# Optimization experiments

Measured on AMD Instinct MI355X. Metric: run time of the kernel, lower is better.

Reference implementation:

```python
import jax, jax.numpy as jnp
import numpy as np

B, C, T, H, F, KS = 8, 512, 1024, 8, 2048, 3
K = C // H            # head channels = 64
ROPE_D = K // 2       # RoPE rotates half the head channels = 32
EPS = 1e-4


def setup_inputs() -> dict:
    key = jax.random.key(0)
    ks = jax.random.split(key, 12)
    s = 1.0 / np.sqrt(C)
    sf = 1.0 / np.sqrt(F)
    return {
        "x": jax.random.normal(ks[0], (B, C, T), jnp.float32),
        "x_mask": jnp.ones((B, 1, T), jnp.float32),
        "attn_mask": jnp.ones((B, 1, T, T), jnp.float32),
        "wq": jax.random.normal(ks[1], (C, C), jnp.float32) * s,
        "bq": jnp.zeros((C,), jnp.float32),
        "wk": jax.random.normal(ks[2], (C, C), jnp.float32) * s,
        "bk": jnp.zeros((C,), jnp.float32),
        "wv": jax.random.normal(ks[3], (C, C), jnp.float32) * s,
        "bv": jnp.zeros((C,), jnp.float32),
        "wo": jax.random.normal(ks[4], (C, C), jnp.float32) * s,
        "bo": jnp.zeros((C,), jnp.float32),
        "w1": jax.random.normal(ks[5], (F, C, KS), jnp.float32) * s,
        "b1": jnp.zeros((F,), jnp.float32),
        "w2": jax.random.normal(ks[6], (C, F, KS), jnp.float32) * sf,
        "b2": jnp.zeros((C,), jnp.float32),
        "g1": jnp.ones((C,), jnp.float32),
        "be1": jnp.zeros((C,), jnp.float32),
        "g2": jnp.ones((C,), jnp.float32),
        "be2": jnp.zeros((C,), jnp.float32),
    }


def _rope(x):
    # x: (B, H, T, K); rotate first ROPE_D channels, pass the rest through.
    t = x.shape[2]
    theta = 1.0 / (10000.0 ** (jnp.arange(0, ROPE_D, 2, dtype=jnp.float32) / ROPE_D))
    idx = jnp.arange(t, dtype=jnp.float32)[:, None] * theta[None, :]  # (T, d/2)
    idx2 = jnp.concatenate([idx, idx], axis=-1)                       # (T, d)
    cos, sin = jnp.cos(idx2), jnp.sin(idx2)                           # broadcast over B,H
    xr, xp = x[..., :ROPE_D], x[..., ROPE_D:]
    h = ROPE_D // 2
    neg = jnp.concatenate([-xr[..., h:], xr[..., :h]], axis=-1)
    return jnp.concatenate([xr * cos + neg * sin, xp], axis=-1)


def _ln(x, gamma, beta):
    # channel-wise LayerNorm over dim 1 of (B, C, T), eps=1e-4
    mean = jnp.mean(x, axis=1, keepdims=True)
    var = jnp.mean((x - mean) ** 2, axis=1, keepdims=True)
    xn = (x - mean) * jax.lax.rsqrt(var + EPS)
    return xn * gamma[None, :, None] + beta[None, :, None]


def _conv1d(x, w, b):
    # x: (B, Cin, T), w: (Cout, Cin, KS), 'same' padding (KS//2)
    y = jax.lax.conv_general_dilated(
        x, w, window_strides=(1,), padding=[(KS // 2, KS // 2)],
        dimension_numbers=("NCH", "OIH", "NCH"))
    return y + b[None, :, None]


def _forward(x, x_mask, attn_mask, wq, bq, wk, bk, wv, bv, wo, bo,
             w1, b1, w2, b2, g1, be1, g2, be2):
    x = x * x_mask
    # 1x1 conv projections == channel matmuls
    q = jnp.einsum("oc,bct->bot", wq, x) + bq[None, :, None]
    k = jnp.einsum("oc,bct->bot", wk, x) + bk[None, :, None]
    v = jnp.einsum("oc,bct->bot", wv, x) + bv[None, :, None]
    # (B, C, T) -> (B, H, T, K)
    def heads(a):
        return a.reshape(B, H, K, T).transpose(0, 1, 3, 2)
    q, k, v = heads(q), heads(k), heads(v)
    q = _rope(q)
    k = _rope(k)
    scores = jnp.einsum("bhtk,bhsk->bhts", q, k) / jnp.sqrt(jnp.float32(K))
    scores = jnp.where(attn_mask == 0, jnp.float32(-10000.0), scores)
    p = jax.nn.softmax(scores, axis=-1)
    o = jnp.einsum("bhts,bhsk->bhtk", p, v)              # (B,H,T,K)
    o = o.transpose(0, 1, 3, 2).reshape(B, C, T)
    y = jnp.einsum("oc,bct->bot", wo, o) + bo[None, :, None]
    x = _ln(x + y, g1, be1)
    # conv FFN
    h1 = jax.nn.relu(_conv1d(x * x_mask, w1, b1))
    y = _conv1d(h1 * x_mask, w2, b2) * x_mask
    x = _ln(x + y, g2, be2)
    return x


def reference(x, x_mask, attn_mask, wq, bq, wk, bk, wv, bv, wo, bo,
              w1, b1, w2, b2, g1, be1, g2, be2):
    return _forward(x, x_mask, attn_mask, wq, bq, wk, bk, wv, bv, wo, bo,
                    w1, b1, w2, b2, g1, be1, g2, be2)
```

## Files before the change

kernel.cpp:

```cpp
#include <hip/hip_runtime.h>

typedef unsigned short u16;
typedef __attribute__((ext_vector_type(4))) float floatx4;
typedef __attribute__((ext_vector_type(8))) __bf16 bf16x8;
typedef __attribute__((ext_vector_type(4))) unsigned short ushort4v;
typedef __attribute__((ext_vector_type(8))) unsigned short ushort8v;

#define DI __device__ __forceinline__


DI u16 f2bf(float f) {
  union { float f; unsigned u; } v; v.f = f;
  unsigned r = v.u + 0x7fffu + ((v.u >> 16) & 1u);
  return (u16)(r >> 16);
}
DI float bf2f(u16 h) {
  union { unsigned u; float f; } v; v.u = ((unsigned)h) << 16;
  return v.f;
}

#define GLDS(g, l) __builtin_amdgcn_global_load_lds( \
    (const __attribute__((address_space(1))) unsigned int*)(g), \
    (__attribute__((address_space(3))) unsigned int*)(l), 16, 0, 0)

__global__ __launch_bounds__(256, 2) void k_fattn(
    const u16* __restrict__ qb, const u16* __restrict__ kb,
    const u16* __restrict__ vb, const unsigned* __restrict__ mb,
    u16* __restrict__ oT)
{
  __shared__ __align__(16) u16 Ps[4][32 * 64];
  const int tid  = threadIdx.x;
  const int wave = tid >> 6, lane = tid & 63;
  const int lr = lane & 15, kg = lane >> 4;
  const int qt = blockIdx.x, bh = blockIdx.y;
  const int bb = bh >> 3, hh = bh & 7;
  const int wq0 = qt * 128 + wave * 32;
  const float L2E = 1.44269504f;

  const u16* Qp = qb + (size_t)bh * 65536;
  const u16* Kp = kb + (size_t)bh * 65536;
  const u16* Vp = vb + (size_t)bh * 65536;
  u16* Pw = &Ps[wave][0];

  bf16x8 qf[2][2];
#pragma unroll
  for (int i = 0; i < 2; ++i)
#pragma unroll
    for (int h = 0; h < 2; ++h)
      qf[i][h] = *(const bf16x8*)&Qp[(wq0 + i * 16 + lr) * 64 + h * 32 + kg * 8];

  float l_b[2] = {0.f, 0.f};
  floatx4 o_acc[2][4];
#pragma unroll
  for (int i = 0; i < 2; ++i)
#pragma unroll
    for (int j = 0; j < 4; ++j) o_acc[i][j] = (floatx4){0.f, 0.f, 0.f, 0.f};

  bf16x8 kf[4][2], vf[4][2];
#pragma unroll
  for (int a = 0; a < 4; ++a)
#pragma unroll
    for (int h = 0; h < 2; ++h)
      kf[a][h] = *(const bf16x8*)&Kp[(a * 16 + lr) * 64 + h * 32 + kg * 8];

  for (int it = 0; it < 16; ++it) {
    const int s0 = it * 64;
    unsigned mw[2][2];
#pragma unroll
    for (int b = 0; b < 2; ++b) {
      const size_t rw = ((size_t)bb << 15) + ((size_t)(wq0 + b * 16 + lr) << 5) + (s0 >> 5);
      mw[b][0] = mb[rw]; mw[b][1] = mb[rw + 1];
    }
    floatx4 sT[4][2];
    __builtin_amdgcn_s_setprio(1);
#pragma unroll
    for (int a = 0; a < 4; ++a) {
      sT[a][0] = (floatx4){0.f, 0.f, 0.f, 0.f};
      sT[a][1] = (floatx4){0.f, 0.f, 0.f, 0.f};
#pragma unroll
      for (int b = 0; b < 2; ++b)
#pragma unroll
        for (int h = 0; h < 2; ++h)
          sT[a][b] = __builtin_amdgcn_mfma_f32_16x16x32_bf16(kf[a][h], qf[b][h], sT[a][b], 0, 0, 0);
    }
    __builtin_amdgcn_s_setprio(0);
#pragma unroll
    for (int a = 0; a < 4; ++a)
#pragma unroll
      for (int h = 0; h < 2; ++h)
        vf[a][h] = *(const bf16x8*)&Vp[(a * 16 + lr) * 1024 + s0 + h * 32 + kg * 8];
    if (it < 15) {
      const int sn = s0 + 64;
#pragma unroll
      for (int a = 0; a < 4; ++a)
#pragma unroll
        for (int h = 0; h < 2; ++h)
          kf[a][h] = *(const bf16x8*)&Kp[(sn + a * 16 + lr) * 64 + h * 32 + kg * 8];
    }
#pragma unroll
    for (int b = 0; b < 2; ++b) {
      float sum = 0.f;
#pragma unroll
      for (int a = 0; a < 4; ++a)
#pragma unroll
        for (int r = 0; r < 4; ++r) {
          const int sl = a * 16 + kg * 4 + r;
          float sv = sT[a][b][r] * 0.125f;
          const unsigned wsel = (sl & 32) ? mw[b][1] : mw[b][0];
          if (!((wsel >> (sl & 31)) & 1u)) sv = -10000.f;
          const float p = exp2f(sv * L2E);
          sT[a][b][r] = p;
          sum += p;
        }
      sum += __shfl_xor(sum, 16);
      sum += __shfl_xor(sum, 32);
      l_b[b] += sum;
#pragma unroll
      for (int a = 0; a < 4; ++a) {
        ushort4v pk;
#pragma unroll
        for (int r = 0; r < 4; ++r) {
          __bf16 hv = (__bf16)sT[a][b][r];
          pk[r] = *(u16*)&hv;
        }
        const int sl0 = a * 16 + kg * 4;
        *(ushort4v*)&Pw[(b * 16 + lr) * 64 + (sl0 ^ ((lr & 7) << 3))] = pk;
      }
    }
    asm volatile("s_waitcnt lgkmcnt(0)" ::: "memory");
    __builtin_amdgcn_sched_barrier(0);
    bf16x8 pa[2][2];
#pragma unroll
    for (int i = 0; i < 2; ++i)
#pragma unroll
      for (int h = 0; h < 2; ++h)
        pa[i][h] = *(const bf16x8*)&Pw[(i * 16 + lr) * 64 + (((h * 4 + kg) ^ (lr & 7)) << 3)];
    __builtin_amdgcn_s_setprio(1);
#pragma unroll
    for (int jd = 0; jd < 4; ++jd)
#pragma unroll
      for (int i = 0; i < 2; ++i)
#pragma unroll
        for (int h = 0; h < 2; ++h)
          o_acc[i][jd] = __builtin_amdgcn_mfma_f32_16x16x32_bf16(pa[i][h], vf[jd][h], o_acc[i][jd], 0, 0, 0);
    __builtin_amdgcn_s_setprio(0);
  }
  float linv[2][4];
#pragma unroll
  for (int i = 0; i < 2; ++i)
#pragma unroll
    for (int r = 0; r < 4; ++r) linv[i][r] = 1.f / __shfl(l_b[i], kg * 4 + r);
#pragma unroll
  for (int i = 0; i < 2; ++i)
#pragma unroll
    for (int jd = 0; jd < 4; ++jd)
#pragma unroll
      for (int r = 0; r < 4; ++r) {
        const int t = wq0 + i * 16 + kg * 4 + r;
        const int c = hh * 64 + jd * 16 + lr;
        oT[((size_t)bb * 1024 + t) * 512 + c] = f2bf(o_acc[i][jd][r] * linv[i][r]);
      }
}

template<int MODE, int BN, int TAPK>
__global__ __launch_bounds__(256) void k_cgemm(
    const u16* __restrict__ A, int lda,
    const u16* __restrict__ Bsrc, int ldb,
    int K,
    u16* __restrict__ o0, u16* __restrict__ o1, u16* __restrict__ o2,
    const float* __restrict__ bias,
    const float* __restrict__ ctab, const float* __restrict__ stab,
    const float* __restrict__ msk)
{
  constexpr int BM = 128;
  constexpr int FN = BN / 32;
  __shared__ __align__(16) u16 As[2 * BM * 32];
  __shared__ __align__(16) u16 Bs[2 * BN * 32];

  const int tid  = threadIdx.x;
  const int wave = tid >> 6, lane = tid & 63;
  const int wm = wave >> 1, wn = wave & 1;
  const int lr = lane & 15, kg = lane >> 4;

  const int nwg = gridDim.x * gridDim.y;
  const int h0  = blockIdx.y * gridDim.x + blockIdx.x;
  const int cpx = nwg >> 3;
  const int tl  = (h0 & 7) * cpx + (h0 >> 3);
  const int bx  = tl % gridDim.x;
  const int by  = tl / gridDim.x;

  const int m0 = bx * BM, n0 = by * BN;
  const int koff = blockIdx.z * K;

  floatx4 acc[4][FN];
#pragma unroll
  for (int i = 0; i < 4; ++i)
#pragma unroll
    for (int j = 0; j < FN; ++j) acc[i][j] = (floatx4){0.f, 0.f, 0.f, 0.f};

  const int csw = (kg ^ ((lr >> 1) & 3)) * 8;

  for (int k0 = 0; k0 < K; k0 += 64) {
#pragma unroll
    for (int h = 0; h < 2; ++h) {
      const int kglob = koff + k0 + h * 32;
#pragma unroll
      for (int ch = 0; ch < BM / 64; ++ch) {
        const int idx = ch * 256 + tid;
        const int row = idx >> 2;
        const int kk = (((idx & 3) ^ ((row >> 1) & 3)) << 3);
        GLDS(A + (size_t)(m0 + row) * lda + (kglob + kk),
             &As[h * BM * 32 + idx * 8]);
      }
#pragma unroll
      for (int ch = 0; ch < BN / 64; ++ch) {
        const int idx = ch * 256 + tid;
        const int row = idx >> 2;
        const int kk = (((idx & 3) ^ ((row >> 1) & 3)) << 3);
        const int bt = n0 + row;
        const u16* src;
        if constexpr (TAPK == 0) {
          src = Bsrc + (size_t)bt * ldb + (kglob + kk);
        } else {
          const int tap = kglob / TAPK, off2 = kglob - tap * TAPK;
          const int b = bt >> 10, t = bt & 1023;
          src = Bsrc + ((size_t)(b * 1026 + t + tap)) * TAPK + off2 + kk;
        }
        GLDS(src, &Bs[h * BN * 32 + idx * 8]);
      }
    }
    __syncthreads();
    bf16x8 af[2][4], bfr[2][FN];
#pragma unroll
    for (int h = 0; h < 2; ++h) {
#pragma unroll
      for (int i = 0; i < 4; ++i)
        af[h][i] = *(const bf16x8*)&As[(h * BM + wm * 64 + i * 16 + lr) * 32 + csw];
#pragma unroll
      for (int j = 0; j < FN; ++j)
        bfr[h][j] = *(const bf16x8*)&Bs[(h * BN + wn * (BN / 2) + j * 16 + lr) * 32 + csw];
    }
#pragma unroll
    for (int h = 0; h < 2; ++h)
#pragma unroll
      for (int i = 0; i < 4; ++i)
#pragma unroll
        for (int j = 0; j < FN; ++j)
          acc[i][j] = __builtin_amdgcn_mfma_f32_16x16x32_bf16(af[h][i], bfr[h][j], acc[i][j], 0, 0, 0);
    __syncthreads();
  }

  const int wrow0 = m0 + wm * 64;
  const int col0  = n0 + wn * (BN / 2);

  if constexpr (MODE == 0) {
    float v[4][FN][4];
#pragma unroll
    for (int i = 0; i < 4; ++i)
#pragma unroll
      for (int j = 0; j < FN; ++j)
#pragma unroll
        for (int r = 0; r < 4; ++r)
          v[i][j][r] = acc[i][j][r] + bias[wrow0 + i * 16 + kg * 4 + r];
    const int sec = wrow0 >> 9;
    const int hh  = (wrow0 & 511) >> 6;
    if (sec < 2) {
#pragma unroll
      for (int j = 0; j < FN; ++j) {
        const int t = (col0 + j * 16 + lr) & 1023;
#pragma unroll
        for (int r = 0; r < 4; ++r) {
          const int a = kg * 4 + r;
          const float cv = ctab[t * 16 + a], sv = stab[t * 16 + a];
          const float a0 = v[0][j][r], a1 = v[1][j][r];
          v[0][j][r] = a0 * cv - a1 * sv;
          v[1][j][r] = a1 * cv + a0 * sv;
        }
      }
      u16* dst = (sec == 0) ? o0 : o1;
#pragma unroll
      for (int i = 0; i < 4; ++i)
#pragma unroll
        for (int j = 0; j < FN; ++j) {
          const int bt = col0 + j * 16 + lr;
          const int b = bt >> 10, t = bt & 1023;
          ushort4v pk;
#pragma unroll
          for (int r = 0; r < 4; ++r) pk[r] = f2bf(v[i][j][r]);
          *(ushort4v*)&dst[(((size_t)b * 8 + hh) * 1024 + t) * 64 + i * 16 + kg * 4] = pk;
        }
    } else {
#pragma unroll
      for (int i = 0; i < 4; ++i)
#pragma unroll
        for (int j = 0; j < FN; ++j) {
          const int bt = col0 + j * 16 + lr;
          const int b = bt >> 10, t = bt & 1023;
#pragma unroll
          for (int r = 0; r < 4; ++r) {
            const int dk = i * 16 + kg * 4 + r;
            o2[(((size_t)b * 8 + hh) * 64 + dk) * 1024 + t] = f2bf(v[i][j][r]);
          }
        }
    }
  } else if constexpr (MODE == 3) {
#pragma unroll
    for (int i = 0; i < 4; ++i)
#pragma unroll
      for (int j = 0; j < FN; ++j) {
        const int bt = col0 + j * 16 + lr;
        const int c0 = wrow0 + i * 16 + kg * 4;
        ushort4v pk;
#pragma unroll
        for (int r = 0; r < 4; ++r) pk[r] = f2bf(acc[i][j][r] + bias[c0 + r]);
        *(ushort4v*)&o0[(size_t)bt * 512 + c0] = pk;
      }
  } else if constexpr (MODE == 4) {
#pragma unroll
    for (int i = 0; i < 4; ++i) {
      const int r0 = wrow0 + i * 16 + kg * 4;
#pragma unroll
      for (int j = 0; j < FN; ++j) {
        const int bt = col0 + j * 16 + lr;
        const int b = bt >> 10, t = bt & 1023;
        const float mv = msk[(size_t)b * 1024 + t];
        ushort4v pk;
#pragma unroll
        for (int r = 0; r < 4; ++r)
          pk[r] = f2bf(fmaxf(acc[i][j][r] + bias[r0 + r], 0.f) * mv);
        *(ushort4v*)&o0[((size_t)(b * 1026 + t + 1)) * 2048 + r0] = pk;
      }
    }
  } else {
    u16* dst = o0 + (size_t)blockIdx.z * 8 * 1024 * 512;
    const bool z0 = (blockIdx.z == 0);
#pragma unroll
    for (int i = 0; i < 4; ++i)
#pragma unroll
      for (int j = 0; j < FN; ++j) {
        const int bt = col0 + j * 16 + lr;
        const int b = bt >> 10, t = bt & 1023;
        const int c0 = wrow0 + i * 16 + kg * 4;
        const float mv = msk[(size_t)b * 1024 + t];
        ushort4v pk;
#pragma unroll
        for (int r = 0; r < 4; ++r) {
          const float bv = z0 ? bias[c0 + r] : 0.f;
          pk[r] = f2bf((acc[i][j][r] + bv) * mv);
        }
        *(ushort4v*)&dst[(size_t)bt * 512 + c0] = pk;
      }
  }
}

__global__ __launch_bounds__(256) void k_prep(
    const float* __restrict__ wq, const float* __restrict__ wk,
    const float* __restrict__ wv, const float* __restrict__ wo,
    const float* __restrict__ w1, const float* __restrict__ w2,
    const float* __restrict__ bq, const float* __restrict__ bk,
    const float* __restrict__ bv, const float* __restrict__ am,
    u16* __restrict__ wqkv, u16* __restrict__ wob,
    u16* __restrict__ w1p, u16* __restrict__ w2p,
    float* __restrict__ bqkv, float* __restrict__ ctab, float* __restrict__ stab,
    unsigned* __restrict__ mbits, u16* __restrict__ x2p, u16* __restrict__ h1p)
{
  const int bid = blockIdx.x;
  if (bid < 4096) {
    const int seg = bid >> 10;
    const int i = (bid & 1023) * 256 + threadIdx.x;
    const float* src = (seg == 0) ? wq : (seg == 1) ? wk : (seg == 2) ? wv : wo;
    u16* dst = (seg < 3) ? (wqkv + (size_t)seg * 512 * 512) : wob;
    dst[i] = f2bf(src[i]);
  } else if (bid < 16384) {
    const int i = (bid - 4096) * 256 + threadIdx.x;
    const int f = i / 1536, rem = i % 1536;
    const int kk = rem >> 9, c = rem & 511;
    w1p[i] = f2bf(w1[f * 1536 + c * 3 + kk]);
  } else if (bid < 28672) {
    const int i = (bid - 16384) * 256 + threadIdx.x;
    const int c = i / 6144, rem = i % 6144;
    const int kk = rem >> 11, f = rem & 2047;
    w2p[i] = f2bf(w2[c * 6144 + f * 3 + kk]);
  } else if (bid < 29696) {
    const int i = (bid - 28672) * 256 + threadIdx.x;
    const float* src = am + (size_t)i * 32;
    unsigned w = 0;
#pragma unroll
    for (int q = 0; q < 32; ++q) w |= (src[q] != 0.f) ? (1u << q) : 0u;
    mbits[i] = w;
  } else if (bid < 29760) {
    const int i = (bid - 29696) * 256 + threadIdx.x;
    const int t = i >> 4, a = i & 15;
    const float theta = powf(10000.f, -(float)a / 16.f);
    const float ang = (float)t * theta;
    ctab[i] = cosf(ang);
    stab[i] = sinf(ang);
  } else if (bid == 29760) {
    for (int i = threadIdx.x; i < 1536; i += 256)
      bqkv[i] = (i < 512) ? bq[i] : (i < 1024) ? bk[i - 512] : bv[i - 1024];
  } else {
    int zb = bid - 29761;
    if (zb < 16) {
      const int b = zb >> 1;
      const size_t row = (zb & 1) ? 1025 : 0;
      u16* r = x2p + ((size_t)b * 1026 + row) * 512;
      for (int i = threadIdx.x; i < 512; i += 256) r[i] = 0;
    } else {
      zb -= 16;
      const int b = zb >> 1;
      const size_t row = (zb & 1) ? 1025 : 0;
      u16* r = h1p + ((size_t)b * 1026 + row) * 2048;
      for (int i = threadIdx.x; i < 2048; i += 256) r[i] = 0;
    }
  }
}

__global__ __launch_bounds__(256) void k_tcvt(const float* __restrict__ in, u16* __restrict__ out,
                                              const float* __restrict__ msk, int R, int TT) {
  __shared__ u16 tile[64][65];
  const int b = blockIdx.z;
  const int r0 = blockIdx.x * 64, t0 = blockIdx.y * 64;
  const int tx = threadIdx.x & 63, ty = threadIdx.x >> 6;
  const float mv = msk ? msk[(size_t)b * TT + t0 + tx] : 1.f;
  const float* ib = in + (size_t)b * R * TT;
#pragma unroll
  for (int rr = ty; rr < 64; rr += 4)
    tile[rr][tx] = f2bf(ib[(size_t)(r0 + rr) * TT + t0 + tx] * mv);
  __syncthreads();
  u16* ob = out + (size_t)b * TT * R;
#pragma unroll
  for (int tt = ty; tt < 64; tt += 4)
    ob[(size_t)(t0 + tt) * R + r0 + tx] = tile[tx][tt];
}

__global__ __launch_bounds__(256) void k_ln1(
    const u16* __restrict__ xbT, const u16* __restrict__ y1T,
    const float* __restrict__ xm, const float* __restrict__ g,
    const float* __restrict__ be, u16* __restrict__ x2T, u16* __restrict__ x2p)
{
  const int lane = threadIdx.x & 63, wv = threadIdx.x >> 6;
  const int row = blockIdx.x * 4 + wv;
  const int b = row >> 10, t = row & 1023;
  const size_t base = (size_t)row * 512 + lane * 8;
  ushort8v ux = *(const ushort8v*)&xbT[base];
  ushort8v uy = *(const ushort8v*)&y1T[base];
  float v[8];
  float sum = 0.f, ss = 0.f;
#pragma unroll
  for (int q = 0; q < 8; ++q) {
    v[q] = bf2f(ux[q]) + bf2f(uy[q]);
    sum += v[q]; ss += v[q] * v[q];
  }
#pragma unroll
  for (int o = 32; o; o >>= 1) { sum += __shfl_xor(sum, o); ss += __shfl_xor(ss, o); }
  const float mean = sum * (1.f / 512.f);
  const float var  = ss * (1.f / 512.f) - mean * mean;
  const float rs   = rsqrtf(var + 1e-4f);
  const float m    = xm[(size_t)b * 1024 + t];
  ushort8v on, om;
#pragma unroll
  for (int q = 0; q < 8; ++q) {
    const int c = lane * 8 + q;
    const float nv = (v[q] - mean) * rs * g[c] + be[c];
    on[q] = f2bf(nv);
    om[q] = f2bf(nv * m);
  }
  *(ushort8v*)&x2T[base] = on;
  *(ushort8v*)&x2p[((size_t)(b * 1026 + t + 1)) * 512 + lane * 8] = om;
}

__global__ __launch_bounds__(256) void k_ln2_stats(
    const u16* __restrict__ x2T, const u16* __restrict__ c2p,
    float2* __restrict__ mr)
{
  constexpr size_t S = (size_t)8 * 1024 * 512;
  const int lane = threadIdx.x & 63, wv = threadIdx.x >> 6;
  const int row = blockIdx.x * 4 + wv;
  const size_t base = (size_t)row * 512 + lane * 8;
  ushort8v u0 = *(const ushort8v*)&x2T[base];
  ushort8v u1 = *(const ushort8v*)&c2p[base];
  ushort8v u2 = *(const ushort8v*)&c2p[S + base];
  ushort8v u3 = *(const ushort8v*)&c2p[2 * S + base];
  ushort8v u4 = *(const ushort8v*)&c2p[3 * S + base];
  float sum = 0.f, ss = 0.f;
#pragma unroll
  for (int q = 0; q < 8; ++q) {
    const float v = bf2f(u0[q]) + bf2f(u1[q]) + bf2f(u2[q]) + bf2f(u3[q]) + bf2f(u4[q]);
    sum += v; ss += v * v;
  }
#pragma unroll
  for (int o = 32; o; o >>= 1) { sum += __shfl_xor(sum, o); ss += __shfl_xor(ss, o); }
  if (lane == 0) {
    const float mean = sum * (1.f / 512.f);
    const float var  = ss * (1.f / 512.f) - mean * mean;
    mr[row] = (float2){mean, rsqrtf(var + 1e-4f)};
  }
}

__global__ __launch_bounds__(256) void k_ln2_write(
    const u16* __restrict__ x2T, const u16* __restrict__ c2p,
    const float2* __restrict__ mr,
    const float* __restrict__ g, const float* __restrict__ be,
    float* __restrict__ out)
{
  constexpr size_t S = (size_t)8 * 1024 * 512;
  __shared__ float tile[64][65];
  const int cc0 = blockIdx.x * 64, t0 = blockIdx.y * 64, b = blockIdx.z;
  const int tid = threadIdx.x;
  const int c4 = (tid & 15) * 4;
  const int tr = tid >> 4;
  float g4[4], b4[4];
#pragma unroll
  for (int q = 0; q < 4; ++q) { g4[q] = g[cc0 + c4 + q]; b4[q] = be[cc0 + c4 + q]; }
#pragma unroll
  for (int it = 0; it < 4; ++it) {
    const int tt = tr + it * 16;
    const int row = b * 1024 + t0 + tt;
    const size_t base = (size_t)row * 512 + cc0 + c4;
    ushort4v u0 = *(const ushort4v*)&x2T[base];
    ushort4v u1 = *(const ushort4v*)&c2p[base];
    ushort4v u2 = *(const ushort4v*)&c2p[S + base];
    ushort4v u3 = *(const ushort4v*)&c2p[2 * S + base];
    ushort4v u4 = *(const ushort4v*)&c2p[3 * S + base];
    const float2 s = mr[row];
#pragma unroll
    for (int q = 0; q < 4; ++q) {
      const float v = bf2f(u0[q]) + bf2f(u1[q]) + bf2f(u2[q]) + bf2f(u3[q]) + bf2f(u4[q]);
      tile[tt][c4 + q] = (v - s.x) * s.y * g4[q] + b4[q];
    }
  }
  __syncthreads();
  const int tx = tid & 63, cg = tid >> 6;
#pragma unroll
  for (int c = cg; c < 64; c += 4)
    out[((size_t)b * 512 + cc0 + c) * 1024 + t0 + tx] = tile[tx][c];
}

extern "C" void kernel_launch(void* const* d_in, const int* in_sizes, int n_in,
                              void* d_out, int out_size, void* d_ws, size_t ws_size,
                              hipStream_t stream) {
  (void)in_sizes; (void)n_in; (void)out_size; (void)ws_size;
  const float* x   = (const float*)d_in[0];
  const float* xm  = (const float*)d_in[1];
  const float* am  = (const float*)d_in[2];
  const float* wq  = (const float*)d_in[3];
  const float* bq  = (const float*)d_in[4];
  const float* wk  = (const float*)d_in[5];
  const float* bk  = (const float*)d_in[6];
  const float* wv  = (const float*)d_in[7];
  const float* bv  = (const float*)d_in[8];
  const float* wo  = (const float*)d_in[9];
  const float* bo  = (const float*)d_in[10];
  const float* w1  = (const float*)d_in[11];
  const float* b1  = (const float*)d_in[12];
  const float* w2  = (const float*)d_in[13];
  const float* b2  = (const float*)d_in[14];
  const float* g1  = (const float*)d_in[15];
  const float* be1 = (const float*)d_in[16];
  const float* g2  = (const float*)d_in[17];
  const float* be2 = (const float*)d_in[18];
  float* out = (float*)d_out;

  char* ws = (char*)d_ws;
  size_t off = 0;
  auto alloc = [&](size_t bytes) { char* p = ws + off; off += (bytes + 255) & ~(size_t)255; return p; };

  u16*   wqkv = (u16*)  alloc((size_t)1536 * 512 * 2);
  u16*   wob  = (u16*)  alloc((size_t)512 * 512 * 2);
  u16*   w1p  = (u16*)  alloc((size_t)2048 * 1536 * 2);
  u16*   w2p  = (u16*)  alloc((size_t)512 * 6144 * 2);
  float* bqkv = (float*)alloc(1536 * 4);
  float* ctab = (float*)alloc(1024 * 16 * 4);
  float* stab = (float*)alloc(1024 * 16 * 4);
  unsigned* mbits = (unsigned*)alloc((size_t)8 * 1024 * 32 * 4);
  float2* mr  = (float2*)alloc((size_t)8192 * 8);
  u16*   x2T  = (u16*)  alloc((size_t)8 * 1024 * 512 * 2);
  u16*   x2p  = (u16*)  alloc((size_t)8 * 1026 * 512 * 2);
  u16*   h1p  = (u16*)  alloc((size_t)8 * 1026 * 2048 * 2);
  u16*   y1T  = (u16*)  alloc((size_t)8 * 1024 * 512 * 2);
  u16*   xbT  = (u16*)  alloc((size_t)8 * 1024 * 512 * 2);
  u16*   oT   = (u16*)  alloc((size_t)8 * 1024 * 512 * 2);
  u16*   qkv3 = (u16*)  alloc((size_t)3 * 8 * 8 * 1024 * 64 * 2);
  u16*   c2p  = (u16*)  alloc((size_t)4 * 8 * 1024 * 512 * 2);

  u16* qb = qkv3;
  u16* kb = qkv3 + (size_t)8 * 8 * 1024 * 64;
  u16* vb = kb   + (size_t)8 * 8 * 1024 * 64;

  dim3 blk(256);

  k_prep<<<dim3(29793), blk, 0, stream>>>(
      wq, wk, wv, wo, w1, w2, bq, bk, bv, am,
      wqkv, wob, w1p, w2p, bqkv, ctab, stab, mbits, x2p, h1p);

  k_tcvt<<<dim3(8, 16, 8), blk, 0, stream>>>(x, xbT, xm, 512, 1024);

  k_cgemm<0, 128, 0><<<dim3(12, 64), blk, 0, stream>>>(
      wqkv, 512, xbT, 512, 512, qb, kb, vb, bqkv, ctab, stab, nullptr);

  k_fattn<<<dim3(8, 64), blk, 0, stream>>>(qb, kb, vb, mbits, oT);

  k_cgemm<3, 64, 0><<<dim3(4, 128), blk, 0, stream>>>(
      wob, 512, oT, 512, 512, y1T, nullptr, nullptr, bo, nullptr, nullptr, nullptr);

  k_ln1<<<dim3(2048), blk, 0, stream>>>(xbT, y1T, xm, g1, be1, x2T, x2p);

  k_cgemm<4, 128, 512><<<dim3(16, 64), blk, 0, stream>>>(
      w1p, 1536, x2p, 0, 1536, h1p, nullptr, nullptr, b1, nullptr, nullptr, xm);
  k_cgemm<5, 128, 2048><<<dim3(4, 64, 4), blk, 0, stream>>>(
      w2p, 6144, h1p, 0, 1536, c2p, nullptr, nullptr, b2, nullptr, nullptr, xm);

  k_ln2_stats<<<dim3(2048), blk, 0, stream>>>(x2T, c2p, mr);
  k_ln2_write<<<dim3(8, 16, 8), blk, 0, stream>>>(x2T, c2p, mr, g2, be2, out);
}
```

Before: 311.3 us.

## Double-buffer GEMM K-loop with async LDS prefetch of next tile

Restructures the cgemm main loop from a synchronous 64-wide K step into a 32-wide K step with two LDS buffers. The next tile's global-to-LDS loads are issued before the current tile is computed, and a partial vmcnt wait lets those loads overlap the MFMAs. It also raises wave priority around the MFMA block. The cost is twice as many barriers per unit of K, and correctness depends on the hand-coded vmcnt counts matching the number of loads issued.

```diff
diff --git a/kernel.cpp b/kernel.cpp
--- a/kernel.cpp
+++ b/kernel.cpp
@@ -174,8 +174,10 @@
 {
   constexpr int BM = 128;
   constexpr int FN = BN / 32;
-  __shared__ __align__(16) u16 As[2 * BM * 32];
-  __shared__ __align__(16) u16 Bs[2 * BN * 32];
+  constexpr int ACH = 2;
+  constexpr int BCH = BN * 32 / (8 * 256);
+  __shared__ __align__(16) u16 As[2][BM * 32];
+  __shared__ __align__(16) u16 Bs[2][BN * 32];
 
   const int tid  = threadIdx.x;
   const int wave = tid >> 6, lane = tid & 63;
@@ -192,6 +194,32 @@
   const int m0 = bx * BM, n0 = by * BN;
   const int koff = blockIdx.z * K;
 
+  auto stage = [&](int buf, int kglob) {
+#pragma unroll
+    for (int ch = 0; ch < ACH; ++ch) {
+      const int idx = ch * 256 + tid;
+      const int row = idx >> 2;
+      const int kk = (((idx & 3) ^ ((row >> 1) & 3)) << 3);
+      GLDS(A + (size_t)(m0 + row) * lda + (kglob + kk), &As[buf][idx * 8]);
+    }
+#pragma unroll
+    for (int ch = 0; ch < BCH; ++ch) {
+      const int idx = ch * 256 + tid;
+      const int row = idx >> 2;
+      const int kk = (((idx & 3) ^ ((row >> 1) & 3)) << 3);
+      const int bt = n0 + row;
+      const u16* src;
+      if constexpr (TAPK == 0) {
+        src = Bsrc + (size_t)bt * ldb + (kglob + kk);
+      } else {
+        const int tap = kglob / TAPK, off2 = kglob - tap * TAPK;
+        const int b = bt >> 10, t = bt & 1023;
+        src = Bsrc + ((size_t)(b * 1026 + t + tap)) * TAPK + off2 + kk;
+      }
+      GLDS(src, &Bs[buf][idx * 8]);
+    }
+  };
+
   floatx4 acc[4][FN];
 #pragma unroll
   for (int i = 0; i < 4; ++i)
@@ -200,54 +228,35 @@
 
   const int csw = (kg ^ ((lr >> 1) & 3)) * 8;
 
-  for (int k0 = 0; k0 < K; k0 += 64) {
-#pragma unroll
-    for (int h = 0; h < 2; ++h) {
-      const int kglob = koff + k0 + h * 32;
-#pragma unroll
-      for (int ch = 0; ch < BM / 64; ++ch) {
-        const int idx = ch * 256 + tid;
-        const int row = idx >> 2;
-        const int kk = (((idx & 3) ^ ((row >> 1) & 3)) << 3);
-        GLDS(A + (size_t)(m0 + row) * lda + (kglob + kk),
-             &As[h * BM * 32 + idx * 8]);
-      }
-#pragma unroll
-      for (int ch = 0; ch < BN / 64; ++ch) {
-        const int idx = ch * 256 + tid;
-        const int row = idx >> 2;
-        const int kk = (((idx & 3) ^ ((row >> 1) & 3)) << 3);
-        const int bt = n0 + row;
-        const u16* src;
-        if constexpr (TAPK == 0) {
-          src = Bsrc + (size_t)bt * ldb + (kglob + kk);
-        } else {
-          const int tap = kglob / TAPK, off2 = kglob - tap * TAPK;
-          const int b = bt >> 10, t = bt & 1023;
-          src = Bsrc + ((size_t)(b * 1026 + t + tap)) * TAPK + off2 + kk;
-        }
-        GLDS(src, &Bs[h * BN * 32 + idx * 8]);
-      }
-    }
-    __syncthreads();
-    bf16x8 af[2][4], bfr[2][FN];
-#pragma unroll
-    for (int h = 0; h < 2; ++h) {
-#pragma unroll
-      for (int i = 0; i < 4; ++i)
-        af[h][i] = *(const bf16x8*)&As[(h * BM + wm * 64 + i * 16 + lr) * 32 + csw];
+  stage(0, koff);
+  int cur = 0;
+  for (int k0 = 0; k0 < K; k0 += 32) {
+    const bool nx = (k0 + 32 < K);
+    if (nx) stage(cur ^ 1, koff + k0 + 32);
+    if (nx) {
+      if constexpr (ACH + BCH == 4) asm volatile("s_waitcnt vmcnt(4)" ::: "memory");
+      else                          asm volatile("s_waitcnt vmcnt(3)" ::: "memory");
+    } else {
+      asm volatile("s_waitcnt vmcnt(0)" ::: "memory");
+    }
+    __builtin_amdgcn_sched_barrier(0);
+    __builtin_amdgcn_s_barrier();
+    bf16x8 af[4], bfr[FN];
+#pragma unroll
+    for (int i = 0; i < 4; ++i)
+      af[i] = *(const bf16x8*)&As[cur][(wm * 64 + i * 16 + lr) * 32 + csw];
+#pragma unroll
+    for (int j = 0; j < FN; ++j)
+      bfr[j] = *(const bf16x8*)&Bs[cur][(wn * (BN / 2) + j * 16 + lr) * 32 + csw];
+    __builtin_amdgcn_s_setprio(1);
+#pragma unroll
+    for (int i = 0; i < 4; ++i)
 #pragma unroll
       for (int j = 0; j < FN; ++j)
-        bfr[h][j] = *(const bf16x8*)&Bs[(h * BN + wn * (BN / 2) + j * 16 + lr) * 32 + csw];
-    }
-#pragma unroll
-    for (int h = 0; h < 2; ++h)
-#pragma unroll
-      for (int i = 0; i < 4; ++i)
-#pragma unroll
-        for (int j = 0; j < FN; ++j)
-          acc[i][j] = __builtin_amdgcn_mfma_f32_16x16x32_bf16(af[h][i], bfr[h][j], acc[i][j], 0, 0, 0);
-    __syncthreads();
+        acc[i][j] = __builtin_amdgcn_mfma_f32_16x16x32_bf16(af[i], bfr[j], acc[i][j], 0, 0, 0);
+    __builtin_amdgcn_s_setprio(0);
+    __builtin_amdgcn_s_barrier();
+    cur ^= 1;
   }
 
   const int wrow0 = m0 + wm * 64;
```

Result: slower. 330.7 us (+6.2%).
